# Kernel optimization log

Hardware: AMD Instinct MI355X
Metric: run time of the kernel (lower is better)

Reference implementation:

```python
import jax, jax.numpy as jnp
import numpy as np

GROUP = 64   # quantization group size (nunchaku W4A4 default)
QMAX = 7.0   # symmetric int4 positive range


def setup_inputs() -> dict:
    key = jax.random.key(0)
    ks = jax.random.split(key, 6)
    T, K, N, R = 256, 3072, 3072, 32
    x = jax.random.normal(ks[0], (T, K), dtype=jnp.float32)
    # int4 weight codes stored as 0..15 (dequant subtracts zero-point 8)
    qweight = jax.random.randint(ks[1], (N, K), 0, 16, dtype=jnp.int32)
    # per-(out_channel, input_group) weight scales, small positive
    wscales = jax.random.uniform(ks[2], (N, K // GROUP), dtype=jnp.float32) * 0.02 + 1e-3
    lora_down = jax.random.normal(ks[3], (R, K), dtype=jnp.float32) / np.sqrt(K)
    lora_up = jax.random.normal(ks[4], (N, R), dtype=jnp.float32) / np.sqrt(R)
    bias = jax.random.normal(ks[5], (N,), dtype=jnp.float32) * 0.01
    return {"x": x, "qweight": qweight, "wscales": wscales,
            "lora_down": lora_down, "lora_up": lora_up, "bias": bias}


def _quantize_act(x):
    # per-token, per-group symmetric int4 fake-quant (quantize -> dequantize)
    T, K = x.shape
    xg = x.reshape(T, K // GROUP, GROUP)
    scale = jnp.maximum(jnp.max(jnp.abs(xg), axis=-1, keepdims=True) / QMAX, 1e-8)
    q = jnp.clip(jnp.round(xg / scale), -8.0, QMAX)
    return (q * scale).reshape(T, K)


def reference(x, qweight, wscales, lora_down, lora_up, bias):
    # Dequantize int4 weights: (code - 8) * per-group scale  -> [N, K]
    N, K = qweight.shape
    w = (qweight.astype(jnp.float32) - 8.0).reshape(N, K // GROUP, GROUP)
    w = (w * wscales[:, :, None]).reshape(N, K)
    # W4A4 main path: int4-quantized activations x dequantized int4 weights
    x_dq = _quantize_act(x)
    main = x_dq @ w.T                               # [T, N]
    # fused low-rank (SVDQuant LoRA) branch on full-precision activations
    lora = (x @ lora_down.T) @ lora_up.T            # [T, R] @ [R, N]
    return main + lora + bias
```

## Files before the change

kernel.cpp:

```cpp
#include <hip/hip_runtime.h>
#include <stdint.h>

#define T_DIM 256
#define K_DIM 3072
#define N_DIM 3072
#define R_DIM 32
#define KG    48
#define NCHUNK 49
#define BN    64
#define NSPLIT 8

typedef __bf16 bf16x8 __attribute__((ext_vector_type(8)));
typedef float  f32x4  __attribute__((ext_vector_type(4)));
typedef unsigned short u16x8 __attribute__((ext_vector_type(8)));

__device__ __forceinline__ unsigned short f2bf(float f) {
    unsigned u = __builtin_bit_cast(unsigned, f);
    unsigned rounding = 0x7FFFu + ((u >> 16) & 1u);
    return (unsigned short)((u + rounding) >> 16);
}

__device__ __forceinline__ bf16x8 cvt8(const float* p) {
    float4 lo = ((const float4*)p)[0], hi = ((const float4*)p)[1];
    u16x8 u;
    u[0] = f2bf(lo.x); u[1] = f2bf(lo.y); u[2] = f2bf(lo.z); u[3] = f2bf(lo.w);
    u[4] = f2bf(hi.x); u[5] = f2bf(hi.y); u[6] = f2bf(hi.z); u[7] = f2bf(hi.w);
    return __builtin_bit_cast(bf16x8, u);
}

__global__ void build_wtail(const float* __restrict__ lora_up,
                            unsigned short* __restrict__ Wt) {
    int idx = blockIdx.x * 256 + threadIdx.x;
    int n = idx >> 6, j = idx & 63;
    float v = (j < R_DIM) ? lora_up[n * R_DIM + j] : 0.f;
    Wt[idx] = f2bf(v);
}

__global__ __launch_bounds__(256) void quant_act(
        const float* __restrict__ x, unsigned short* __restrict__ Ap) {
    int widx = blockIdx.x * 4 + (threadIdx.x >> 6);
    int lane = threadIdx.x & 63;
    int t = widx / KG, g = widx % KG;
    float v = x[(size_t)t * K_DIM + g * 64 + lane];
    float a = fabsf(v);
    #pragma unroll
    for (int off = 32; off; off >>= 1) a = fmaxf(a, __shfl_xor(a, off));
    float scale = fmaxf(a / 7.0f, 1e-8f);
    float q = rintf(v / scale);
    q = fminf(fmaxf(q, -8.f), 7.f);
    Ap[((size_t)g * T_DIM + t) * 64 + lane] = f2bf(q * scale);
}

__global__ __launch_bounds__(256) void lora_mid(
        const float* __restrict__ x, const float* __restrict__ lora_down,
        float* __restrict__ Lm) {
    int kb = blockIdx.x;
    int lane = threadIdx.x & 63, wv = threadIdx.x >> 6;
    int mrow = lane & 15, quad = lane >> 4;
    f32x4 acc[4][2];
    f32x4 zero = {0.f, 0.f, 0.f, 0.f};
    #pragma unroll
    for (int i = 0; i < 4; ++i) { acc[i][0] = zero; acc[i][1] = zero; }
    #pragma unroll
    for (int ki = 0; ki < 6; ++ki) {
        int k0 = kb * 192 + ki * 32 + quad * 8;
        bf16x8 a[4], b[2];
        #pragma unroll
        for (int mt = 0; mt < 4; ++mt)
            a[mt] = cvt8(x + (size_t)(wv * 64 + mt * 16 + mrow) * K_DIM + k0);
        #pragma unroll
        for (int nt = 0; nt < 2; ++nt)
            b[nt] = cvt8(lora_down + (size_t)(nt * 16 + mrow) * K_DIM + k0);
        #pragma unroll
        for (int mt = 0; mt < 4; ++mt)
            #pragma unroll
            for (int nt = 0; nt < 2; ++nt)
                acc[mt][nt] = __builtin_amdgcn_mfma_f32_16x16x32_bf16(
                    a[mt], b[nt], acc[mt][nt], 0, 0, 0);
    }
    #pragma unroll
    for (int mt = 0; mt < 4; ++mt)
        #pragma unroll
        for (int nt = 0; nt < 2; ++nt)
            #pragma unroll
            for (int r = 0; r < 4; ++r)
                atomicAdd(&Lm[(size_t)(wv * 64 + mt * 16 + quad * 4 + r) * R_DIM
                              + nt * 16 + mrow], acc[mt][nt][r]);
}

__global__ void pack_lora(const float* __restrict__ Lm,
                          unsigned short* __restrict__ Ap) {
    int idx = blockIdx.x * 256 + threadIdx.x;
    int t = idx >> 6, j = idx & 63;
    float v = (j < R_DIM) ? Lm[t * R_DIM + j] : 0.f;
    Ap[((size_t)48 * T_DIM + t) * 64 + j] = f2bf(v);
}

__global__ __launch_bounds__(256) void gemm_main(
        const unsigned short* __restrict__ Ap,
        const int*            __restrict__ qweight,
        const float*          __restrict__ wscales,
        const unsigned short* __restrict__ Wt,
        const float*          __restrict__ bias,
        float*                __restrict__ out) {
    __shared__ short As[T_DIM * 64];
    __shared__ short Bs[BN * 64];
    int nblk  = blockIdx.x;
    int split = blockIdx.y;
    int c0 = split * 6;
    int c1 = (split == NSPLIT - 1) ? NCHUNK : c0 + 6;
    int tid = threadIdx.x;
    int lane = tid & 63, wv = tid >> 6;
    int mrow = lane & 15, quad = lane >> 4;
    int n_row = tid >> 2, seg = tid & 3;
    const int nbase = nblk * BN;

    f32x4 acc[4][4];
    f32x4 zero = {0.f, 0.f, 0.f, 0.f};
    #pragma unroll
    for (int i = 0; i < 4; ++i)
        #pragma unroll
        for (int j = 0; j < 4; ++j) acc[i][j] = zero;

    for (int kt = c0; kt < c1; ++kt) {
        __syncthreads();
        {
            const uint4* gA = (const uint4*)(Ap + (size_t)kt * (T_DIM * 64)) + tid * 8;
            uint4* sA = ((uint4*)As) + tid * 8;
            #pragma unroll
            for (int i = 0; i < 8; ++i) sA[i] = gA[i];
        }
        if (kt < 48) {
            const int* gq = qweight + (size_t)(nbase + n_row) * K_DIM + kt * 64 + seg * 16;
            float wsv = wscales[(nbase + n_row) * KG + kt];
            int4 c[4];
            #pragma unroll
            for (int i = 0; i < 4; ++i) c[i] = ((const int4*)gq)[i];
            const int* ci = (const int*)c;
            alignas(16) unsigned short wb[16];
            #pragma unroll
            for (int j = 0; j < 16; ++j) wb[j] = f2bf((float)(ci[j] - 8) * wsv);
            uint4* sB = (uint4*)&Bs[n_row * 64 + seg * 16];
            sB[0] = ((const uint4*)wb)[0];
            sB[1] = ((const uint4*)wb)[1];
        } else {
            const uint4* gw = (const uint4*)(Wt + (size_t)(nbase + n_row) * 64) + seg * 2;
            uint4* sB = (uint4*)&Bs[n_row * 64 + seg * 16];
            sB[0] = gw[0];
            sB[1] = gw[1];
        }
        __syncthreads();
        #pragma unroll
        for (int ks = 0; ks < 64; ks += 32) {
            bf16x8 a[4], b[4];
            #pragma unroll
            for (int mt = 0; mt < 4; ++mt)
                a[mt] = *(const bf16x8*)&As[(wv * 64 + mt * 16 + mrow) * 64 + ks + quad * 8];
            #pragma unroll
            for (int nt = 0; nt < 4; ++nt)
                b[nt] = *(const bf16x8*)&Bs[(nt * 16 + mrow) * 64 + ks + quad * 8];
            #pragma unroll
            for (int mt = 0; mt < 4; ++mt)
                #pragma unroll
                for (int nt = 0; nt < 4; ++nt)
                    acc[mt][nt] = __builtin_amdgcn_mfma_f32_16x16x32_bf16(
                        a[mt], b[nt], acc[mt][nt], 0, 0, 0);
        }
    }
    #pragma unroll
    for (int nt = 0; nt < 4; ++nt) {
        int n = nbase + nt * 16 + mrow;
        float bv = (split == NSPLIT - 1) ? bias[n] : 0.f;
        #pragma unroll
        for (int mt = 0; mt < 4; ++mt) {
            int row0 = wv * 64 + mt * 16 + quad * 4;
            #pragma unroll
            for (int r = 0; r < 4; ++r)
                atomicAdd(&out[(size_t)(row0 + r) * N_DIM + n], acc[mt][nt][r] + bv);
        }
    }
}

extern "C" void kernel_launch(void* const* d_in, const int* in_sizes, int n_in,
                              void* d_out, int out_size, void* d_ws, size_t ws_size,
                              hipStream_t stream) {
    const float* x         = (const float*)d_in[0];
    const int*   qweight   = (const int*)d_in[1];
    const float* wscales   = (const float*)d_in[2];
    const float* lora_down = (const float*)d_in[3];
    const float* lora_up   = (const float*)d_in[4];
    const float* bias      = (const float*)d_in[5];
    float* out = (float*)d_out;

    char* wsp = (char*)d_ws;
    unsigned short* Ap = (unsigned short*)wsp;
    wsp += (size_t)NCHUNK * T_DIM * 64 * 2;
    unsigned short* Wt = (unsigned short*)wsp;
    wsp += (size_t)N_DIM * 64 * 2;
    float* Lm = (float*)wsp;

    hipMemsetAsync(d_out, 0, (size_t)T_DIM * N_DIM * sizeof(float), stream);
    hipMemsetAsync(Lm, 0, (size_t)T_DIM * R_DIM * sizeof(float), stream);
    build_wtail<<<(N_DIM * 64) / 256, 256, 0, stream>>>(lora_up, Wt);
    quant_act<<<(T_DIM * KG) / 4, 256, 0, stream>>>(x, Ap);
    lora_mid<<<16, 256, 0, stream>>>(x, lora_down, Lm);
    pack_lora<<<(T_DIM * 64) / 256, 256, 0, stream>>>(Lm, Ap);
    gemm_main<<<dim3(48, NSPLIT), 256, 0, stream>>>(Ap, qweight, wscales, Wt, bias, out);
}
```

Baseline: 143.3 us.

## Double-buffer GEMM tiles with async global-to-LDS loads and k-major layout

The main GEMM now double-buffers its LDS tiles. Activation and LoRA tiles are loaded with global_load_lds directly into shared memory, and int4 weight codes are prefetched two chunks ahead in registers, so the next tile's loads overlap the current MFMA work and one barrier per iteration is removed. The activation and LoRA-up workspaces are relaid into a k-major 8-element interleaved layout to match the direct LDS copy and the fragment reads. The lora_mid kernel is also spread over many more blocks, one 32-wide K slice each, at the cost of more atomics. Together these add register pressure, double the LDS footprint and make correctness depend on the new barrier ordering.

After: 140.6 us. About the same (-1.8%).

```diff
diff --git a/kernel.cpp b/kernel.cpp
--- a/kernel.cpp
+++ b/kernel.cpp
@@ -7,7 +7,6 @@
 #define R_DIM 32
 #define KG    48
 #define NCHUNK 49
-#define BN    64
 #define NSPLIT 8
 
 typedef __bf16 bf16x8 __attribute__((ext_vector_type(8)));
@@ -28,12 +27,20 @@
     return __builtin_bit_cast(bf16x8, u);
 }
 
+__device__ __forceinline__ void glds16(const void* gptr, void* lptr) {
+    __builtin_amdgcn_global_load_lds(
+        (const __attribute__((address_space(1))) unsigned int*)gptr,
+        (__attribute__((address_space(3))) unsigned int*)lptr,
+        16, 0, 0);
+}
+
 __global__ void build_wtail(const float* __restrict__ lora_up,
                             unsigned short* __restrict__ Wt) {
     int idx = blockIdx.x * 256 + threadIdx.x;
     int n = idx >> 6, j = idx & 63;
+    int nblk = n >> 6, nl = n & 63;
     float v = (j < R_DIM) ? lora_up[n * R_DIM + j] : 0.f;
-    Wt[idx] = f2bf(v);
+    Wt[(((size_t)nblk * 8 + (j >> 3)) * 64 + nl) * 8 + (j & 7)] = f2bf(v);
 }
 
 __global__ __launch_bounds__(256) void quant_act(
@@ -48,36 +55,32 @@
     float scale = fmaxf(a / 7.0f, 1e-8f);
     float q = rintf(v / scale);
     q = fminf(fmaxf(q, -8.f), 7.f);
-    Ap[((size_t)g * T_DIM + t) * 64 + lane] = f2bf(q * scale);
+    Ap[(((size_t)g * 8 + (lane >> 3)) * 256 + t) * 8 + (lane & 7)] = f2bf(q * scale);
 }
 
 __global__ __launch_bounds__(256) void lora_mid(
         const float* __restrict__ x, const float* __restrict__ lora_down,
         float* __restrict__ Lm) {
-    int kb = blockIdx.x;
     int lane = threadIdx.x & 63, wv = threadIdx.x >> 6;
     int mrow = lane & 15, quad = lane >> 4;
+    int k0 = blockIdx.x * 32 + quad * 8;
+    bf16x8 a[4], b[2];
+    #pragma unroll
+    for (int mt = 0; mt < 4; ++mt)
+        a[mt] = cvt8(x + (size_t)(wv * 64 + mt * 16 + mrow) * K_DIM + k0);
+    #pragma unroll
+    for (int nt = 0; nt < 2; ++nt)
+        b[nt] = cvt8(lora_down + (size_t)(nt * 16 + mrow) * K_DIM + k0);
     f32x4 acc[4][2];
     f32x4 zero = {0.f, 0.f, 0.f, 0.f};
     #pragma unroll
     for (int i = 0; i < 4; ++i) { acc[i][0] = zero; acc[i][1] = zero; }
     #pragma unroll
-    for (int ki = 0; ki < 6; ++ki) {
-        int k0 = kb * 192 + ki * 32 + quad * 8;
-        bf16x8 a[4], b[2];
-        #pragma unroll
-        for (int mt = 0; mt < 4; ++mt)
-            a[mt] = cvt8(x + (size_t)(wv * 64 + mt * 16 + mrow) * K_DIM + k0);
+    for (int mt = 0; mt < 4; ++mt)
         #pragma unroll
         for (int nt = 0; nt < 2; ++nt)
-            b[nt] = cvt8(lora_down + (size_t)(nt * 16 + mrow) * K_DIM + k0);
-        #pragma unroll
-        for (int mt = 0; mt < 4; ++mt)
-            #pragma unroll
-            for (int nt = 0; nt < 2; ++nt)
-                acc[mt][nt] = __builtin_amdgcn_mfma_f32_16x16x32_bf16(
-                    a[mt], b[nt], acc[mt][nt], 0, 0, 0);
-    }
+            acc[mt][nt] = __builtin_amdgcn_mfma_f32_16x16x32_bf16(
+                a[mt], b[nt], acc[mt][nt], 0, 0, 0);
     #pragma unroll
     for (int mt = 0; mt < 4; ++mt)
         #pragma unroll
@@ -93,18 +96,18 @@
     int idx = blockIdx.x * 256 + threadIdx.x;
     int t = idx >> 6, j = idx & 63;
     float v = (j < R_DIM) ? Lm[t * R_DIM + j] : 0.f;
-    Ap[((size_t)48 * T_DIM + t) * 64 + j] = f2bf(v);
+    Ap[((size_t)(384 + (j >> 3)) * 256 + t) * 8 + (j & 7)] = f2bf(v);
 }
 
 __global__ __launch_bounds__(256) void gemm_main(
-        const unsigned short* __restrict__ Ap,
+        const uint4*          __restrict__ ApU,
         const int*            __restrict__ qweight,
         const float*          __restrict__ wscales,
-        const unsigned short* __restrict__ Wt,
+        const uint4*          __restrict__ WtU,
         const float*          __restrict__ bias,
         float*                __restrict__ out) {
-    __shared__ short As[T_DIM * 64];
-    __shared__ short Bs[BN * 64];
+    __shared__ uint4 AsU[2][2048];
+    __shared__ uint4 BsU[2][512];
     int nblk  = blockIdx.x;
     int split = blockIdx.y;
     int c0 = split * 6;
@@ -113,7 +116,9 @@
     int lane = tid & 63, wv = tid >> 6;
     int mrow = lane & 15, quad = lane >> 4;
     int n_row = tid >> 2, seg = tid & 3;
-    const int nbase = nblk * BN;
+    const int nbase = nblk * 64;
+    const int* qrow = qweight + (size_t)(nbase + n_row) * K_DIM + seg * 16;
+    const float* wsrow = wscales + (size_t)(nbase + n_row) * KG;
 
     f32x4 acc[4][4];
     f32x4 zero = {0.f, 0.f, 0.f, 0.f};
@@ -122,43 +127,63 @@
         #pragma unroll
         for (int j = 0; j < 4; ++j) acc[i][j] = zero;
 
+    int4 bc[2][4];
+    float wsr[2];
+
+    {
+        const uint4* gA = ApU + (size_t)c0 * 2048;
+        #pragma unroll
+        for (int i = 0; i < 8; ++i)
+            glds16(&gA[tid + i * 256], &AsU[0][tid + i * 256]);
+        const int4* g0 = (const int4*)(qrow + c0 * 64);
+        const int4* g1 = (const int4*)(qrow + (c0 + 1) * 64);
+        #pragma unroll
+        for (int i = 0; i < 4; ++i) { bc[0][i] = g0[i]; bc[1][i] = g1[i]; }
+        wsr[0] = wsrow[c0];
+        wsr[1] = wsrow[c0 + 1];
+    }
+
     for (int kt = c0; kt < c1; ++kt) {
+        int lc = kt - c0;
+        int p = lc & 1;
+        if (kt < 48) {
+            float w = wsr[p];
+            const int* ci = (const int*)bc[p];
+            alignas(16) unsigned short wb[16];
+            #pragma unroll
+            for (int j = 0; j < 16; ++j) wb[j] = f2bf((float)(ci[j] - 8) * w);
+            const uint4* w2 = (const uint4*)wb;
+            BsU[p][(seg * 2 + 0) * 64 + n_row] = w2[0];
+            BsU[p][(seg * 2 + 1) * 64 + n_row] = w2[1];
+        }
         __syncthreads();
-        {
-            const uint4* gA = (const uint4*)(Ap + (size_t)kt * (T_DIM * 64)) + tid * 8;
-            uint4* sA = ((uint4*)As) + tid * 8;
-            #pragma unroll
-            for (int i = 0; i < 8; ++i) sA[i] = gA[i];
-        }
-        if (kt < 48) {
-            const int* gq = qweight + (size_t)(nbase + n_row) * K_DIM + kt * 64 + seg * 16;
-            float wsv = wscales[(nbase + n_row) * KG + kt];
-            int4 c[4];
-            #pragma unroll
-            for (int i = 0; i < 4; ++i) c[i] = ((const int4*)gq)[i];
-            const int* ci = (const int*)c;
-            alignas(16) unsigned short wb[16];
-            #pragma unroll
-            for (int j = 0; j < 16; ++j) wb[j] = f2bf((float)(ci[j] - 8) * wsv);
-            uint4* sB = (uint4*)&Bs[n_row * 64 + seg * 16];
-            sB[0] = ((const uint4*)wb)[0];
-            sB[1] = ((const uint4*)wb)[1];
-        } else {
-            const uint4* gw = (const uint4*)(Wt + (size_t)(nbase + n_row) * 64) + seg * 2;
-            uint4* sB = (uint4*)&Bs[n_row * 64 + seg * 16];
-            sB[0] = gw[0];
-            sB[1] = gw[1];
-        }
-        __syncthreads();
-        #pragma unroll
-        for (int ks = 0; ks < 64; ks += 32) {
+        if (kt + 2 < c1 && kt + 2 < 48) {
+            const int4* gq = (const int4*)(qrow + (kt + 2) * 64);
+            #pragma unroll
+            for (int i = 0; i < 4; ++i) bc[p][i] = gq[i];
+            wsr[p] = wsrow[kt + 2];
+        }
+        if (kt + 1 < c1) {
+            const uint4* gA = ApU + (size_t)(kt + 1) * 2048;
+            #pragma unroll
+            for (int i = 0; i < 8; ++i)
+                glds16(&gA[tid + i * 256], &AsU[p ^ 1][tid + i * 256]);
+            if (kt + 1 == 48) {
+                #pragma unroll
+                for (int j = 0; j < 2; ++j)
+                    glds16(&WtU[(size_t)nblk * 512 + tid + j * 256],
+                           &BsU[p ^ 1][tid + j * 256]);
+            }
+        }
+        #pragma unroll
+        for (int ks8 = 0; ks8 < 8; ks8 += 4) {
             bf16x8 a[4], b[4];
             #pragma unroll
             for (int mt = 0; mt < 4; ++mt)
-                a[mt] = *(const bf16x8*)&As[(wv * 64 + mt * 16 + mrow) * 64 + ks + quad * 8];
+                a[mt] = *(const bf16x8*)&AsU[p][(quad + ks8) * 256 + wv * 64 + mt * 16 + mrow];
             #pragma unroll
             for (int nt = 0; nt < 4; ++nt)
-                b[nt] = *(const bf16x8*)&Bs[(nt * 16 + mrow) * 64 + ks + quad * 8];
+                b[nt] = *(const bf16x8*)&BsU[p][(quad + ks8) * 64 + nt * 16 + mrow];
             #pragma unroll
             for (int mt = 0; mt < 4; ++mt)
                 #pragma unroll
@@ -194,16 +219,17 @@
 
     char* wsp = (char*)d_ws;
     unsigned short* Ap = (unsigned short*)wsp;
-    wsp += (size_t)NCHUNK * T_DIM * 64 * 2;
+    wsp += (size_t)NCHUNK * 2048 * 16;
     unsigned short* Wt = (unsigned short*)wsp;
-    wsp += (size_t)N_DIM * 64 * 2;
+    wsp += (size_t)48 * 512 * 16;
     float* Lm = (float*)wsp;
 
     hipMemsetAsync(d_out, 0, (size_t)T_DIM * N_DIM * sizeof(float), stream);
     hipMemsetAsync(Lm, 0, (size_t)T_DIM * R_DIM * sizeof(float), stream);
     build_wtail<<<(N_DIM * 64) / 256, 256, 0, stream>>>(lora_up, Wt);
     quant_act<<<(T_DIM * KG) / 4, 256, 0, stream>>>(x, Ap);
-    lora_mid<<<16, 256, 0, stream>>>(x, lora_down, Lm);
+    lora_mid<<<K_DIM / 32, 256, 0, stream>>>(x, lora_down, Lm);
     pack_lora<<<(T_DIM * 64) / 256, 256, 0, stream>>>(Lm, Ap);
-    gemm_main<<<dim3(48, NSPLIT), 256, 0, stream>>>(Ap, qweight, wscales, Wt, bias, out);
-}
+    gemm_main<<<dim3(48, NSPLIT), 256, 0, stream>>>(
+        (const uint4*)Ap, qweight, wscales, (const uint4*)Wt, bias, out);
+}
```
